# Kernel optimization log

Measured on AMD Instinct MI355X. Metric: run time of the kernel, lower is better.

The kernel has to match this reference:

```python
import jax, jax.numpy as jnp
import numpy as np

B, L, NB = 8192, 40, 2        # batch, maxlen, behavior features
V, E = 100000, 64             # vocab per table, embed dim per table
NS, ND = 3, 8                 # other sparse feats, dense feats
D = NB * E                    # concatenated behavior embed dim = 128
ALL = D + D + (ND + NS * E)   # info_all dim = 456
NEG_INF = -2.0**32 + 1
BN_EPS = 1e-3                 # keras BatchNormalization default epsilon


def setup_inputs() -> dict:
    key = jax.random.key(0)
    ks = jax.random.split(key, 20)
    inp = {
        "dense_inputs": jax.random.normal(ks[0], (B, ND), jnp.float32),
        "sparse_inputs": jax.random.randint(ks[1], (B, NS), 0, V),
        "seq_inputs": jax.random.randint(ks[2], (B, L, NB), 0, V),
        "item_inputs": jax.random.randint(ks[3], (B, NB), 0, V),
        # embedding tables (random_uniform init in keras)
        "emb_sparse": jax.random.uniform(ks[4], (NS, V, E), jnp.float32, -0.05, 0.05),
        "emb_seq": jax.random.uniform(ks[5], (NB, V, E), jnp.float32, -0.05, 0.05),
        # attention MLP: input 4*D=512 -> 80 -> 40 -> 1
        "att_W1": jax.random.normal(ks[6], (4 * D, 80), jnp.float32) * 0.05,
        "att_b1": jnp.zeros((80,), jnp.float32),
        "att_W2": jax.random.normal(ks[7], (80, 40), jnp.float32) * 0.05,
        "att_b2": jnp.zeros((40,), jnp.float32),
        "att_Wf": jax.random.normal(ks[8], (40, 1), jnp.float32) * 0.05,
        "att_bf": jnp.zeros((1,), jnp.float32),
        # batch norm (inference-mode moving stats)
        "bn_gamma": jnp.ones((ALL,), jnp.float32),
        "bn_beta": jnp.zeros((ALL,), jnp.float32),
        "bn_mean": jnp.zeros((ALL,), jnp.float32),
        "bn_var": jnp.ones((ALL,), jnp.float32),
        # FFN: ALL -> 80 -> 40 -> 1, PReLU alphas per-feature
        "ffn_W1": jax.random.normal(ks[9], (ALL, 80), jnp.float32) * 0.05,
        "ffn_b1": jnp.zeros((80,), jnp.float32),
        "ffn_a1": jnp.full((80,), 0.25, jnp.float32),
        "ffn_W2": jax.random.normal(ks[10], (80, 40), jnp.float32) * 0.05,
        "ffn_b2": jnp.zeros((40,), jnp.float32),
        "ffn_a2": jnp.full((40,), 0.25, jnp.float32),
        "out_W": jax.random.normal(ks[11], (40, 1), jnp.float32) * 0.05,
        "out_b": jnp.zeros((1,), jnp.float32),
    }
    return inp


def prelu(x, alpha):
    return jnp.where(x > 0, x, alpha * x)


def reference(dense_inputs, sparse_inputs, seq_inputs, item_inputs,
              emb_sparse, emb_seq,
              att_W1, att_b1, att_W2, att_b2, att_Wf, att_bf,
              bn_gamma, bn_beta, bn_mean, bn_var,
              ffn_W1, ffn_b1, ffn_a1, ffn_W2, ffn_b2, ffn_a2,
              out_W, out_b):
    mask = (seq_inputs[:, :, 0] != 0)                                   # [B, L]
    # other sparse embeddings + dense features
    other_info = jnp.concatenate(
        [dense_inputs] + [emb_sparse[i][sparse_inputs[:, i]] for i in range(NS)], axis=-1)
    # behavior sequence / candidate item embeddings
    seq_embed = jnp.concatenate([emb_seq[i][seq_inputs[:, :, i]] for i in range(NB)], axis=-1)  # [B,L,D]
    item_embed = jnp.concatenate([emb_seq[i][item_inputs[:, i]] for i in range(NB)], axis=-1)   # [B,D]

    # local activation attention
    q = jnp.broadcast_to(item_embed[:, None, :], seq_embed.shape)       # [B,L,D]
    info = jnp.concatenate([q, seq_embed, q - seq_embed, q * seq_embed], axis=-1)  # [B,L,4D]
    h = jax.nn.sigmoid(info @ att_W1 + att_b1)
    h = jax.nn.sigmoid(h @ att_W2 + att_b2)
    logits = (h @ att_Wf + att_bf)[..., 0]                               # [B,L]
    logits = jnp.where(mask, logits, NEG_INF)
    att = jax.nn.softmax(logits, axis=-1)                                # [B,L]
    user_info = jnp.einsum('bl,bld->bd', att, seq_embed)                 # [B,D]

    info_all = jnp.concatenate([user_info, item_embed, other_info], axis=-1)  # [B,ALL]
    info_all = bn_gamma * (info_all - bn_mean) * jax.lax.rsqrt(bn_var + BN_EPS) + bn_beta
    info_all = prelu(info_all @ ffn_W1 + ffn_b1, ffn_a1)
    info_all = prelu(info_all @ ffn_W2 + ffn_b2, ffn_a2)
    return jax.nn.sigmoid(info_all @ out_W + out_b)                      # [B,1]
```

## Files before the change

### kernel.cpp

```cpp
#include <hip/hip_runtime.h>

#define BB 8192
#define LL 40
#define VV 100000
#define NEG_INF_F (-4294967295.0f)
#define XS 264
#define HS 104
#define XGS 480

typedef __attribute__((ext_vector_type(8))) short short8;
typedef __attribute__((ext_vector_type(4))) float f32x4;

__device__ __forceinline__ unsigned short f2bf(float f) {
  unsigned u = __float_as_uint(f);
  u += 0x7FFFu + ((u >> 16) & 1u);
  return (unsigned short)(u >> 16);
}
__device__ __forceinline__ float bf2f(unsigned short s) {
  return __uint_as_float(((unsigned)s) << 16);
}

__global__ void prep_all(const float* __restrict__ W1, float* __restrict__ wqcT,
                         unsigned short* __restrict__ WsdpT,
                         const float* __restrict__ aW2, unsigned short* __restrict__ W2bT,
                         const float* __restrict__ fW2, unsigned short* __restrict__ W2fT,
                         const float* __restrict__ fW1, const float* __restrict__ g,
                         const float* __restrict__ vr, unsigned short* __restrict__ W1fT,
                         const float* __restrict__ fb1, const float* __restrict__ be,
                         const float* __restrict__ mn, float* __restrict__ b1p) {
  __shared__ float red[4];
  int bid = blockIdx.x, t = threadIdx.x;
  if (bid < 40) {
    int i = bid * 256 + t;
    int h = i >> 7, k = i & 127;
    float a = W1[k * 80 + h];
    float b = W1[(128 + k) * 80 + h];
    float c = W1[(256 + k) * 80 + h];
    float d = W1[(384 + k) * 80 + h];
    wqcT[h * 132 + k] = a + c;
    WsdpT[h * 256 + k] = f2bf(b - c);
    WsdpT[h * 256 + 128 + k] = f2bf(d);
  } else if (bid < 58) {
    int i = (bid - 40) * 256 + t;
    int n = i / 96, k = i % 96;
    W2bT[i] = (n < 40 && k < 80) ? f2bf(aW2[k * 40 + n]) : (unsigned short)0;
  } else if (bid < 76) {
    int i = (bid - 58) * 256 + t;
    int n = i / 96, k = i % 96;
    W2fT[i] = (n < 40 && k < 80) ? f2bf(fW2[k * 40 + n]) : (unsigned short)0;
  } else if (bid < 226) {
    int i = (bid - 76) * 256 + t;
    int n = i / 480, k = i % 480;
    float v = 0.f;
    if (k < 456) v = fW1[k * 80 + n] * g[k] * rsqrtf(vr[k] + 1e-3f);
    W1fT[i] = f2bf(v);
  } else {
    int n = bid - 226;
    float p = 0.f;
    for (int k = t; k < 456; k += 256) {
      float sc = g[k] * rsqrtf(vr[k] + 1e-3f);
      p += (be[k] - mn[k] * sc) * fW1[k * 80 + n];
    }
    for (int off = 32; off; off >>= 1) p += __shfl_xor(p, off, 64);
    if ((t & 63) == 0) red[t >> 6] = p;
    __syncthreads();
    if (t == 0) b1p[n] = fb1[n] + red[0] + red[1] + red[2] + red[3];
  }
}


__launch_bounds__(256, 3)
__global__ void din_att(const float* __restrict__ dense, const int* __restrict__ sparsei,
                        const int* __restrict__ seqi, const int* __restrict__ itemi,
                        const float* __restrict__ embS, const float* __restrict__ embQ,
                        const float* __restrict__ wqcT, const unsigned short* __restrict__ WsdpT,
                        const unsigned short* __restrict__ W2bT,
                        const float* __restrict__ ab1, const float* __restrict__ ab2,
                        const float* __restrict__ aWf, const float* __restrict__ abf,
                        unsigned short* __restrict__ Xg) {
  __shared__ __align__(16) unsigned short sX[48 * XS];
  __shared__ __align__(16) unsigned short sH1[48 * HS];
  __shared__ float sQ[128];
  __shared__ float sQC[80];
  __shared__ float sOther[200];
  __shared__ float sH2T[40 * 41];
  __shared__ float sAtt[40];

  const int t = threadIdx.x;
  const int b = blockIdx.x;
  const int wv = t >> 6, ln = t & 63, m16 = ln & 15, quad = ln >> 4;

  short8 Bf[8];
  {
    const unsigned short* br = WsdpT + (size_t)(wv * 16 + m16) * 256 + quad * 8;
#pragma unroll
    for (int kt = 0; kt < 8; kt++) Bf[kt] = *(const short8*)(br + kt * 32);
  }

  if (t < 32) {
    int f = t >> 4, sub = t & 15;
    int idx = itemi[b * 2 + f];
    float4 v = *(const float4*)(embQ + ((size_t)(f * VV + idx)) * 64 + sub * 4);
    *(float4*)(sQ + f * 64 + sub * 4) = v;
  } else if (t < 80) {
    int j = t - 32, f = j >> 4, sub = j & 15;
    int idx = sparsei[b * 3 + f];
    float4 v = *(const float4*)(embS + ((size_t)(f * VV + idx)) * 64 + sub * 4);
    *(float4*)(sOther + 8 + f * 64 + sub * 4) = v;
  } else if (t < 88) {
    sOther[t - 80] = dense[b * 8 + (t - 80)];
  }
  for (int i = t; i < 1280; i += 256) {
    int r = i >> 4, sub = i & 15;
    int l = r >> 1, f = r & 1;
    int idx = seqi[b * 80 + r];
    float4 v = *(const float4*)(embQ + ((size_t)(f * VV + idx)) * 64 + sub * 4);
    ushort4 u;
    u.x = f2bf(v.x); u.y = f2bf(v.y); u.z = f2bf(v.z); u.w = f2bf(v.w);
    *(ushort4*)(sX + l * XS + f * 64 + sub * 4) = u;
  }
  for (int i = t; i < 384; i += 256) {
    int r = i >> 3, c = i & 7;
    ((unsigned*)sH1)[r * 52 + 40 + c] = 0u;
  }
  __syncthreads();

  if (t < 80) {
    float acc = ab1[t];
    const float* wq = wqcT + t * 132;
    for (int k = 0; k < 128; k += 4) {
      float4 w = *(const float4*)(wq + k);
      float4 q = *(const float4*)(sQ + k);
      acc += q.x * w.x + q.y * w.y + q.z * w.z + q.w * w.w;
    }
    sQC[t] = acc;
  } else {
    for (int i = t - 80; i < 2560; i += 176) {
      int l = i >> 6, kp = i & 63;
      unsigned sv = *(const unsigned*)(sX + l * XS + 2 * kp);
      float s0 = bf2f((unsigned short)sv);
      float s1 = bf2f((unsigned short)(sv >> 16));
      float p0 = sQ[2 * kp] * s0, p1 = sQ[2 * kp + 1] * s1;
      *(unsigned*)(sX + l * XS + 128 + 2 * kp) =
          (unsigned)f2bf(p0) | ((unsigned)f2bf(p1) << 16);
    }
  }
  __syncthreads();

  {
    const int h = wv * 16 + m16;
    const float qc = sQC[h];
#pragma unroll
    for (int mt = 0; mt < 3; mt++) {
      f32x4 acc = {0.f, 0.f, 0.f, 0.f};
      const unsigned short* ar = sX + (mt * 16 + m16) * XS + quad * 8;
#pragma unroll
      for (int kt = 0; kt < 8; kt++) {
        short8 a = *(const short8*)(ar + kt * 32);
        acc = __builtin_amdgcn_mfma_f32_16x16x32_bf16(a, Bf[kt], acc, 0, 0, 0);
      }
#pragma unroll
      for (int r = 0; r < 4; r++) {
        int l = mt * 16 + quad * 4 + r;
        float z = acc[r] + qc;
        sH1[l * HS + h] = f2bf(1.f / (1.f + __expf(-z)));
      }
    }
    if (wv < 3) {
      short8 B4[8];
      const unsigned short* br = WsdpT + (size_t)(64 + m16) * 256 + quad * 8;
#pragma unroll
      for (int kt = 0; kt < 8; kt++) B4[kt] = *(const short8*)(br + kt * 32);
      f32x4 acc = {0.f, 0.f, 0.f, 0.f};
      const unsigned short* ar = sX + (wv * 16 + m16) * XS + quad * 8;
#pragma unroll
      for (int kt = 0; kt < 8; kt++) {
        short8 a = *(const short8*)(ar + kt * 32);
        acc = __builtin_amdgcn_mfma_f32_16x16x32_bf16(a, B4[kt], acc, 0, 0, 0);
      }
      int h4 = 64 + m16;
      float qc4 = sQC[h4];
#pragma unroll
      for (int r = 0; r < 4; r++) {
        int l = wv * 16 + quad * 4 + r;
        float z = acc[r] + qc4;
        sH1[l * HS + h4] = f2bf(1.f / (1.f + __expf(-z)));
      }
    }
  }
  __syncthreads();

  for (int tile = wv; tile < 9; tile += 4) {
    int mt = tile / 3, nt = tile % 3;
    f32x4 acc = {0.f, 0.f, 0.f, 0.f};
    const unsigned short* ar = sH1 + (mt * 16 + m16) * HS + quad * 8;
    const unsigned short* br = W2bT + (nt * 16 + m16) * 96 + quad * 8;
#pragma unroll
    for (int kt = 0; kt < 3; kt++) {
      short8 a = *(const short8*)(ar + kt * 32);
      short8 bb = *(const short8*)(br + kt * 32);
      acc = __builtin_amdgcn_mfma_f32_16x16x32_bf16(a, bb, acc, 0, 0, 0);
    }
    int j = nt * 16 + m16;
    if (j < 40) {
      float b2 = ab2[j];
#pragma unroll
      for (int r = 0; r < 4; r++) {
        int l = mt * 16 + quad * 4 + r;
        if (l < 40) sH2T[j * 41 + l] = 1.f / (1.f + __expf(-(acc[r] + b2)));
      }
    }
  }
  __syncthreads();

  if (wv == 0) {
    float logit = -3.0e38f;
    if (t < 40) {
      float acc = abf[0];
      for (int j = 0; j < 40; j++) acc += sH2T[j * 41 + t] * aWf[j];
      logit = (seqi[b * 80 + 2 * t] != 0) ? acc : NEG_INF_F;
    }
    float mx = logit;
    for (int off = 32; off; off >>= 1) mx = fmaxf(mx, __shfl_xor(mx, off, 64));
    float ex = (t < 40) ? __expf(logit - mx) : 0.f;
    float sm = ex;
    for (int off = 32; off; off >>= 1) sm += __shfl_xor(sm, off, 64);
    if (t < 40) sAtt[t] = ex / sm;
  } else {
    int j = t - 64;
    unsigned* xr = (unsigned*)(Xg + (size_t)b * XGS);
    if (j < 64) {
      xr[64 + j] = (unsigned)f2bf(sQ[2 * j]) | ((unsigned)f2bf(sQ[2 * j + 1]) << 16);
    } else if (j < 164) {
      int p = j - 64;
      xr[128 + p] = (unsigned)f2bf(sOther[2 * p]) | ((unsigned)f2bf(sOther[2 * p + 1]) << 16);
    } else if (j < 176) {
      xr[228 + (j - 164)] = 0u;
    }
  }
  __syncthreads();

  if (t < 128) {
    float acc = 0.f;
    for (int l = 0; l < 40; l++) acc += sAtt[l] * bf2f(sX[l * XS + t]);
    Xg[(size_t)b * XGS + t] = f2bf(acc);
  }
}


__launch_bounds__(256, 3)
__global__ void din_ffn(const unsigned short* __restrict__ Xg,
                        const unsigned short* __restrict__ W1fT, const float* __restrict__ b1p,
                        const float* __restrict__ fa1,
                        const unsigned short* __restrict__ W2fT, const float* __restrict__ fb2,
                        const float* __restrict__ fa2,
                        const float* __restrict__ oW, const float* __restrict__ ob,
                        float* __restrict__ out) {
  __shared__ __align__(16) unsigned short sXB[16 * 488];
  __shared__ __align__(16) unsigned short sH1B[16 * HS];
  __shared__ float sH2B[16 * 41];
  const int t = threadIdx.x, blk = blockIdx.x;
  const int wv = t >> 6, ln = t & 63, m16 = ln & 15, quad = ln >> 4;

  short8 Bf[15];
  {
    const unsigned short* br = W1fT + (size_t)(wv * 16 + m16) * 480 + quad * 8;
#pragma unroll
    for (int kt = 0; kt < 15; kt++) Bf[kt] = *(const short8*)(br + kt * 32);
  }

  for (int i = t; i < 960; i += 256) {
    int r = i / 60, c = i % 60;
    *(uint4*)(sXB + r * 488 + c * 8) =
        *(const uint4*)(Xg + (size_t)(blk * 16 + r) * XGS + c * 8);
  }
  if (t < 128) {
    int r = t >> 3, c = t & 7;
    ((unsigned*)sH1B)[r * 52 + 40 + c] = 0u;
  }
  __syncthreads();

  {
    int h = wv * 16 + m16;
    f32x4 acc = {0.f, 0.f, 0.f, 0.f};
    const unsigned short* ar = sXB + m16 * 488 + quad * 8;
#pragma unroll
    for (int kt = 0; kt < 15; kt++) {
      short8 a = *(const short8*)(ar + kt * 32);
      acc = __builtin_amdgcn_mfma_f32_16x16x32_bf16(a, Bf[kt], acc, 0, 0, 0);
    }
    float b1v = b1p[h], a1v = fa1[h];
#pragma unroll
    for (int r = 0; r < 4; r++) {
      int l = quad * 4 + r;
      float z = acc[r] + b1v;
      z = z > 0.f ? z : a1v * z;
      sH1B[l * HS + h] = f2bf(z);
    }
    if (wv == 0) {
      short8 B4[15];
      const unsigned short* br = W1fT + (size_t)(64 + m16) * 480 + quad * 8;
#pragma unroll
      for (int kt = 0; kt < 15; kt++) B4[kt] = *(const short8*)(br + kt * 32);
      f32x4 acc4 = {0.f, 0.f, 0.f, 0.f};
#pragma unroll
      for (int kt = 0; kt < 15; kt++) {
        short8 a = *(const short8*)(ar + kt * 32);
        acc4 = __builtin_amdgcn_mfma_f32_16x16x32_bf16(a, B4[kt], acc4, 0, 0, 0);
      }
      int h4 = 64 + m16;
      float b1v4 = b1p[h4], a1v4 = fa1[h4];
#pragma unroll
      for (int r = 0; r < 4; r++) {
        int l = quad * 4 + r;
        float z = acc4[r] + b1v4;
        z = z > 0.f ? z : a1v4 * z;
        sH1B[l * HS + h4] = f2bf(z);
      }
    }
  }
  __syncthreads();

  if (wv < 3) {
    f32x4 acc = {0.f, 0.f, 0.f, 0.f};
    const unsigned short* ar = sH1B + m16 * HS + quad * 8;
    const unsigned short* br = W2fT + (wv * 16 + m16) * 96 + quad * 8;
#pragma unroll
    for (int kt = 0; kt < 3; kt++) {
      short8 a = *(const short8*)(ar + kt * 32);
      short8 bb = *(const short8*)(br + kt * 32);
      acc = __builtin_amdgcn_mfma_f32_16x16x32_bf16(a, bb, acc, 0, 0, 0);
    }
    int j = wv * 16 + m16;
    if (j < 40) {
      float b2 = fb2[j], a2 = fa2[j];
#pragma unroll
      for (int r = 0; r < 4; r++) {
        int l = quad * 4 + r;
        float z = acc[r] + b2;
        sH2B[l * 41 + j] = z > 0.f ? z : a2 * z;
      }
    }
  }
  __syncthreads();

  if (t < 16) {
    float acc = ob[0];
    for (int j = 0; j < 40; j++) acc += sH2B[t * 41 + j] * oW[j];
    out[blk * 16 + t] = 1.f / (1.f + __expf(-acc));
  }
}


extern "C" void kernel_launch(void* const* d_in, const int* in_sizes, int n_in,
                              void* d_out, int out_size, void* d_ws, size_t ws_size,
                              hipStream_t stream) {
  const float* dense  = (const float*)d_in[0];
  const int*   sparsei = (const int*)d_in[1];
  const int*   seqi   = (const int*)d_in[2];
  const int*   itemi  = (const int*)d_in[3];
  const float* embS   = (const float*)d_in[4];
  const float* embQ   = (const float*)d_in[5];
  const float* aW1    = (const float*)d_in[6];
  const float* ab1    = (const float*)d_in[7];
  const float* aW2    = (const float*)d_in[8];
  const float* ab2    = (const float*)d_in[9];
  const float* aWf    = (const float*)d_in[10];
  const float* abf    = (const float*)d_in[11];
  const float* bng    = (const float*)d_in[12];
  const float* bnb    = (const float*)d_in[13];
  const float* bnm    = (const float*)d_in[14];
  const float* bnv    = (const float*)d_in[15];
  const float* fW1    = (const float*)d_in[16];
  const float* fb1    = (const float*)d_in[17];
  const float* fa1    = (const float*)d_in[18];
  const float* fW2    = (const float*)d_in[19];
  const float* fb2    = (const float*)d_in[20];
  const float* fa2    = (const float*)d_in[21];
  const float* oW     = (const float*)d_in[22];
  const float* ob     = (const float*)d_in[23];
  float* out = (float*)d_out;

  float* ws = (float*)d_ws;
  float* wqcT = ws;
  float* b1p  = ws + 10560;
  unsigned short* WsdpT = (unsigned short*)(ws + 10640);
  unsigned short* W2bT  = (unsigned short*)(ws + 20880);
  unsigned short* W2fT  = (unsigned short*)(ws + 23184);
  unsigned short* W1fT  = (unsigned short*)(ws + 25488);
  unsigned short* Xg    = (unsigned short*)(ws + 44688);

  prep_all<<<306, 256, 0, stream>>>(aW1, wqcT, WsdpT, aW2, W2bT, fW2, W2fT,
                                    fW1, bng, bnv, W1fT, fb1, bnb, bnm, b1p);
  din_att<<<BB, 256, 0, stream>>>(dense, sparsei, seqi, itemi, embS, embQ,
                                  wqcT, WsdpT, W2bT, ab1, ab2, aWf, abf, Xg);
  din_ffn<<<512, 256, 0, stream>>>(Xg, W1fT, b1p, fa1, W2fT, fb2, fa2, oW, ob, out);
}
```

Measured before the change: 365.6 us.

## Shrink attention kernel LDS by fusing final logit dot into layer-2 epilogue

```diff
diff --git a/kernel.cpp b/kernel.cpp
--- a/kernel.cpp
+++ b/kernel.cpp
@@ -69,7 +69,7 @@
 }
 
 
-__launch_bounds__(256, 3)
+__launch_bounds__(256, 5)
 __global__ void din_att(const float* __restrict__ dense, const int* __restrict__ sparsei,
                         const int* __restrict__ seqi, const int* __restrict__ itemi,
                         const float* __restrict__ embS, const float* __restrict__ embQ,
@@ -78,13 +78,14 @@
                         const float* __restrict__ ab1, const float* __restrict__ ab2,
                         const float* __restrict__ aWf, const float* __restrict__ abf,
                         unsigned short* __restrict__ Xg) {
-  __shared__ __align__(16) unsigned short sX[48 * XS];
-  __shared__ __align__(16) unsigned short sH1[48 * HS];
-  __shared__ float sQ[128];
-  __shared__ float sQC[80];
-  __shared__ float sOther[200];
-  __shared__ float sH2T[40 * 41];
-  __shared__ float sAtt[40];
+  __shared__ __align__(16) char smem[31392];
+  unsigned short* sX  = (unsigned short*)smem;
+  unsigned short* sH1 = (unsigned short*)smem + 10560;
+  float* sQ     = (float*)(smem + 29440);
+  float* sQC    = sQ + 128;
+  float* sOther = sQC + 80;
+  float* sAtt   = sOther + 200;
+  float* sLogit = sAtt + 40;
 
   const int t = threadIdx.x;
   const int b = blockIdx.x;
@@ -109,6 +110,8 @@
     *(float4*)(sOther + 8 + f * 64 + sub * 4) = v;
   } else if (t < 88) {
     sOther[t - 80] = dense[b * 8 + (t - 80)];
+  } else if (t < 128) {
+    sLogit[t - 88] = 0.f;
   }
   for (int i = t; i < 1280; i += 256) {
     int r = i >> 4, sub = i & 15;
@@ -119,7 +122,7 @@
     u.x = f2bf(v.x); u.y = f2bf(v.y); u.z = f2bf(v.z); u.w = f2bf(v.w);
     *(ushort4*)(sX + l * XS + f * 64 + sub * 4) = u;
   }
-  for (int i = t; i < 384; i += 256) {
+  for (int i = t; i < 320; i += 256) {
     int r = i >> 3, c = i & 7;
     ((unsigned*)sH1)[r * 52 + 40 + c] = 0u;
   }
@@ -162,8 +165,10 @@
 #pragma unroll
       for (int r = 0; r < 4; r++) {
         int l = mt * 16 + quad * 4 + r;
-        float z = acc[r] + qc;
-        sH1[l * HS + h] = f2bf(1.f / (1.f + __expf(-z)));
+        if (l < 40) {
+          float z = acc[r] + qc;
+          sH1[l * HS + h] = f2bf(1.f / (1.f + __expf(-z)));
+        }
       }
     }
     if (wv < 3) {
@@ -183,8 +188,10 @@
 #pragma unroll
       for (int r = 0; r < 4; r++) {
         int l = wv * 16 + quad * 4 + r;
-        float z = acc[r] + qc4;
-        sH1[l * HS + h4] = f2bf(1.f / (1.f + __expf(-z)));
+        if (l < 40) {
+          float z = acc[r] + qc4;
+          sH1[l * HS + h4] = f2bf(1.f / (1.f + __expf(-z)));
+        }
       }
     }
   }
@@ -202,12 +209,24 @@
       acc = __builtin_amdgcn_mfma_f32_16x16x32_bf16(a, bb, acc, 0, 0, 0);
     }
     int j = nt * 16 + m16;
-    if (j < 40) {
-      float b2 = ab2[j];
+    float b2 = (j < 40) ? ab2[j] : 0.f;
+    float wf = (j < 40) ? aWf[j] : 0.f;
+    float c[4];
+#pragma unroll
+    for (int r = 0; r < 4; r++) {
+      float h2 = 1.f / (1.f + __expf(-(acc[r] + b2)));
+      c[r] = (j < 40) ? h2 * wf : 0.f;
+    }
+#pragma unroll
+    for (int off = 1; off < 16; off <<= 1) {
+#pragma unroll
+      for (int r = 0; r < 4; r++) c[r] += __shfl_xor(c[r], off, 64);
+    }
+    if (m16 == 0) {
 #pragma unroll
       for (int r = 0; r < 4; r++) {
         int l = mt * 16 + quad * 4 + r;
-        if (l < 40) sH2T[j * 41 + l] = 1.f / (1.f + __expf(-(acc[r] + b2)));
+        if (l < 40) atomicAdd(&sLogit[l], c[r]);
       }
     }
   }
@@ -216,9 +235,7 @@
   if (wv == 0) {
     float logit = -3.0e38f;
     if (t < 40) {
-      float acc = abf[0];
-      for (int j = 0; j < 40; j++) acc += sH2T[j * 41 + t] * aWf[j];
-      logit = (seqi[b * 80 + 2 * t] != 0) ? acc : NEG_INF_F;
+      logit = (seqi[b * 80 + 2 * t] != 0) ? (sLogit[t] + abf[0]) : NEG_INF_F;
     }
     float mx = logit;
     for (int off = 32; off; off >>= 1) mx = fmaxf(mx, __shfl_xor(mx, off, 64));
@@ -248,7 +265,7 @@
 }
 
 
-__launch_bounds__(256, 3)
+__launch_bounds__(256, 2)
 __global__ void din_ffn(const unsigned short* __restrict__ Xg,
                         const unsigned short* __restrict__ W1fT, const float* __restrict__ b1p,
                         const float* __restrict__ fa1,
```

Measured after the change: 328.1 us. 1.11x faster.
